# Performance work log

Measured on AMD Instinct MI355X. Metric: run time of the kernel, lower is better.

The kernel has to match this reference:

```python
import jax, jax.numpy as jnp
import numpy as np

EPS = 1e-5

def _hdc_branch(emb, w, b, dil, ln_g, ln_b):
    # emb: [N, L, E]; w: [K, E, F] ('WIO'); same-length dilated conv
    y = jax.lax.conv_general_dilated(
        emb, w, window_strides=(1,), padding=[(dil, dil)],
        rhs_dilation=(dil,), dimension_numbers=('NWC', 'WIO', 'NWC')) + b
    m = y.mean(-1, keepdims=True)
    v = ((y - m) ** 2).mean(-1, keepdims=True)
    y = (y - m) / jnp.sqrt(v + EPS) * ln_g + ln_b
    return jax.nn.relu(y)  # [N, L, F]

def _news_encoder(titles, embedding, w1, b1, w2, b2, w3, b3, ln_g, ln_b,
                  q_levels, q_words):
    B, n, L = titles.shape
    E = embedding.shape[-1]
    emb = embedding[titles].reshape(B * n, L, E)  # dropout = identity (eval)
    d = jnp.stack([
        _hdc_branch(emb, w1, b1, 1, ln_g, ln_b),
        _hdc_branch(emb, w2, b2, 2, ln_g, ln_b),
        _hdc_branch(emb, w3, b3, 3, ln_g, ln_b),
    ], axis=2)  # [Bn, L, 3, F]
    F = d.shape[-1]
    d = d.reshape(B, n, L, 3, F)
    scale = jnp.sqrt(jnp.asarray(E, d.dtype))  # original divides by sqrt(embedding_dim)
    # level-wise attention pooling (1-row query over 3 levels)
    wl = jax.nn.softmax(jnp.einsum('f,bnlkf->bnlk', q_levels[0], d) / scale, axis=-1)
    attn = jnp.einsum('bnlk,bnlkf->bnlf', wl, d)  # [B, n, L, F]
    # word-wise attention pooling (1-row query over L words)
    ww = jax.nn.softmax(jnp.einsum('f,bnlf->bnl', q_words[0], attn) / scale, axis=-1)
    reprs = jnp.einsum('bnl,bnlf->bnf', ww, attn)  # [B, n, F]
    return reprs

def setup_inputs() -> dict:
    key = jax.random.key(0)
    ks = jax.random.split(key, 12)
    V, E, F, H = 50000, 300, 150, 50
    return {
        'candidate_title': jax.random.randint(ks[0], (64, 5, 30), 0, V),
        'clicked_title': jax.random.randint(ks[1], (64, H, 30), 0, V),
        'embedding': jax.random.normal(ks[2], (V, E), jnp.float32),
        'w1': jax.random.normal(ks[3], (3, E, F), jnp.float32) * 0.05,
        'b1': jax.random.normal(ks[4], (F,), jnp.float32) * 0.05,
        'w2': jax.random.normal(ks[5], (3, E, F), jnp.float32) * 0.05,
        'b2': jax.random.normal(ks[6], (F,), jnp.float32) * 0.05,
        'w3': jax.random.normal(ks[7], (3, E, F), jnp.float32) * 0.05,
        'b3': jax.random.normal(ks[8], (F,), jnp.float32) * 0.05,
        'ln_g': jnp.ones((F,), jnp.float32),
        'ln_b': jnp.zeros((F,), jnp.float32),
        'q_levels': jax.random.normal(ks[9], (1, F), jnp.float32),
        'q_words': jax.random.normal(ks[10], (1, F), jnp.float32),
        'ltr_w': jax.random.normal(ks[11], (1, H), jnp.float32) * 0.1,
        'ltr_b': jnp.zeros((1,), jnp.float32),
    }

def reference(candidate_title, clicked_title, embedding, w1, b1, w2, b2, w3, b3,
              ln_g, ln_b, q_levels, q_words, ltr_w, ltr_b):
    cdd = _news_encoder(candidate_title, embedding, w1, b1, w2, b2, w3, b3,
                        ln_g, ln_b, q_levels, q_words)  # [B, cdd, F]
    his = _news_encoder(clicked_title, embedding, w1, b1, w2, b2, w3, b3,
                        ln_g, ln_b, q_levels, q_words)  # [B, his, F]
    scores = jnp.einsum('bcf,bhf->bch', cdd, his)        # [B, cdd, his]
    logits = jnp.einsum('bch,oh->bco', scores, ltr_w)[..., 0] + ltr_b[0]  # [B, cdd]
    return jax.nn.log_softmax(logits, axis=1)  # cdd_size > 1 branch
```

## Files before the change

### kernel.cpp

```cpp
#include <hip/hip_runtime.h>

typedef unsigned short u16;
typedef unsigned int   u32;
typedef __bf16 bf16x8 __attribute__((ext_vector_type(8)));
typedef float  f32x4  __attribute__((ext_vector_type(4)));
typedef _Float16 h2 __attribute__((ext_vector_type(2)));

#define M_ROWS 50000
#define M_PAD  50176
#define M_TILES 196
#define N_REAL 1368
#define N_PAD  1536
#define N_TILES64 22
#define K_DIM  300
#define K_PAD  320
#define KT     10
#define TROW   1408
#define SEG    152
#define YCOL   152

#define GLDS(gp, lp) __builtin_amdgcn_global_load_lds( \
    (const __attribute__((address_space(1))) void*)(gp), \
    (__attribute__((address_space(3))) void*)(lp), 16, 0, 0)

static __device__ __forceinline__ u16 f2bf(float x){
  union { float f; u32 u; } a; a.f = x;
  u32 r = a.u + 0x7fffu + ((a.u >> 16) & 1u);
  return (u16)(r >> 16);
}
static __device__ __forceinline__ u16 f2h(float x){
  _Float16 h = (_Float16)x;
  u16 r; __builtin_memcpy(&r, &h, 2); return r;
}
static __device__ __forceinline__ float h2f(u16 v){
  _Float16 h; __builtin_memcpy(&h, &v, 2); return (float)h;
}

static __device__ __forceinline__ float wsum63(float x){
  asm volatile(
    "s_nop 1\n\t"
    "v_add_f32 %0, %0, %0 row_shr:1 bound_ctrl:0\n\t"
    "s_nop 1\n\t"
    "v_add_f32 %0, %0, %0 row_shr:2 bound_ctrl:0\n\t"
    "s_nop 1\n\t"
    "v_add_f32 %0, %0, %0 row_shr:4 bound_ctrl:0\n\t"
    "s_nop 1\n\t"
    "v_add_f32 %0, %0, %0 row_shr:8 bound_ctrl:0\n\t"
    "s_nop 1\n\t"
    "v_add_f32 %0, %0, %0 row_bcast:15 row_mask:0xa\n\t"
    "s_nop 1\n\t"
    "v_add_f32 %0, %0, %0 row_bcast:31 row_mask:0xc\n\t"
    "s_nop 1"
    : "+v"(x));
  return x;
}
static __device__ __forceinline__ float wmax63(float x){
  asm volatile(
    "s_nop 1\n\t"
    "v_max_f32 %0, %0, %0 row_shr:1\n\t"
    "s_nop 1\n\t"
    "v_max_f32 %0, %0, %0 row_shr:2\n\t"
    "s_nop 1\n\t"
    "v_max_f32 %0, %0, %0 row_shr:4\n\t"
    "s_nop 1\n\t"
    "v_max_f32 %0, %0, %0 row_shr:8\n\t"
    "s_nop 1\n\t"
    "v_max_f32 %0, %0, %0 row_bcast:15 row_mask:0xa\n\t"
    "s_nop 1\n\t"
    "v_max_f32 %0, %0, %0 row_bcast:31 row_mask:0xc\n\t"
    "s_nop 1"
    : "+v"(x));
  return x;
}
static __device__ __forceinline__ float rdl63(float x){
  union { float f; int i; } a; a.f = x;
  union { int i; float f; } r; r.i = __builtin_amdgcn_readlane(a.i, 63);
  return r.f;
}

__global__ __launch_bounds__(256) void build_A(const float* __restrict__ emb, u16* __restrict__ A){
  int t = blockIdx.x * 256 + threadIdx.x;
  if (t >= M_PAD * 40) return;
  int m = t / 40, kg = t % 40;
  int k0 = kg * 8;
  int kt = kg >> 2, kgl = kg & 3;
  int tile = m >> 8, ml = m & 255, mb = ml >> 4, row = ml & 15;
  size_t off = ((size_t)tile * KT + kt) * 8192 + mb * 512 + kgl * 128 + row * 8;
  union { uint4 q; u16 s[8]; } p;
  if (m < M_ROWS && k0 + 8 <= K_DIM){
    const float4* src = (const float4*)(emb + (size_t)m * K_DIM + k0);
    float4 v0 = src[0], v1 = src[1];
    p.s[0] = f2bf(v0.x); p.s[1] = f2bf(v0.y); p.s[2] = f2bf(v0.z); p.s[3] = f2bf(v0.w);
    p.s[4] = f2bf(v1.x); p.s[5] = f2bf(v1.y); p.s[6] = f2bf(v1.z); p.s[7] = f2bf(v1.w);
  } else {
    #pragma unroll
    for (int j = 0; j < 8; ++j){
      int k = k0 + j;
      float x = (m < M_ROWS && k < K_DIM) ? emb[(size_t)m * K_DIM + k] : 0.f;
      p.s[j] = f2bf(x);
    }
  }
  *(uint4*)(A + off) = p.q;
}

__global__ void build_B(const float* __restrict__ w1, const float* __restrict__ w2,
                        const float* __restrict__ w3, u16* __restrict__ B){
  int t = blockIdx.x * 256 + threadIdx.x;
  if (t >= N_PAD * K_PAD) return;
  int n = t / K_PAD, k = t % K_PAD;
  float x = 0.f;
  if (n < N_REAL && k < K_DIM){
    int br = n / 456, rem = n % 456, tap = rem / 152, f = rem % 152;
    if (f < 150){
      const float* w = (br == 0) ? w1 : ((br == 1) ? w2 : w3);
      x = w[(tap * K_DIM + k) * 150 + f];
    }
  }
  int tn = n >> 7, nl = n & 127, nb = nl >> 4, col = nl & 15;
  int kt = k >> 5, kl = k & 31, kg = kl >> 3, k8 = kl & 7;
  B[((size_t)tn * KT + kt) * 4096 + nb * 512 + kg * 128 + col * 8 + k8] = f2bf(x);
}

__global__ __launch_bounds__(256, 5) void gemm_k(const u16* __restrict__ A, const u16* __restrict__ B,
                                                 u16* __restrict__ T){
  __shared__ __align__(16) u16 lds[6144];
  const int flat = blockIdx.x;
  const int xcd = flat & 7, ord = flat >> 3;
  const int wg = xcd * 1078 + ord;
  const int tn = wg % 22, tM = wg / 22;
  const int t256 = tM >> 1, hM = tM & 1;
  const int tn128 = tn >> 1, h64 = tn & 1;
  const int tid = threadIdx.x, wave = tid >> 6, lane = tid & 63;
  const int wm = wave >> 1, wn = wave & 1;
  f32x4 acc[4][2];
  #pragma unroll
  for (int i = 0; i < 4; ++i)
    #pragma unroll
    for (int j = 0; j < 2; ++j) acc[i][j] = (f32x4){0.f, 0.f, 0.f, 0.f};
  const u16* Ab = A + ((size_t)t256 * KT) * 8192 + hM * 4096;
  const u16* Bb = B + ((size_t)tn128 * KT) * 4096 + h64 * 2048;
  #pragma unroll
  for (int s = 0; s < 10; ++s){
    __syncthreads();
    GLDS(Ab + s * 8192 + tid * 8,        lds + tid * 8);
    GLDS(Ab + s * 8192 + 2048 + tid * 8, lds + 2048 + tid * 8);
    GLDS(Bb + s * 4096 + tid * 8,        lds + 4096 + tid * 8);
    __syncthreads();
    const bf16x8* A8 = (const bf16x8*)lds;
    const bf16x8* B8 = (const bf16x8*)(lds + 4096);
    bf16x8 av[4], bv[2];
    #pragma unroll
    for (int i = 0; i < 4; ++i) av[i] = A8[(wm * 4 + i) * 64 + lane];
    #pragma unroll
    for (int j = 0; j < 2; ++j) bv[j] = B8[(wn * 2 + j) * 64 + lane];
    #pragma unroll
    for (int i = 0; i < 4; ++i)
      #pragma unroll
      for (int j = 0; j < 2; ++j)
        acc[i][j] = __builtin_amdgcn_mfma_f32_16x16x32_bf16(av[i], bv[j], acc[i][j], 0, 0, 0);
  }
  const int r0 = (lane >> 4) * 4, c0 = lane & 15;
  const int row = tid >> 2, q = tid & 3;
  #pragma unroll
  for (int h = 0; h < 2; ++h){
    __syncthreads();
    if (wm == h){
      #pragma unroll
      for (int i = 0; i < 4; ++i){
        #pragma unroll
        for (int j = 0; j < 2; ++j){
          int col = wn * 32 + j * 16 + c0;
          #pragma unroll
          for (int r = 0; r < 4; ++r)
            lds[(i * 16 + r0 + r) * 72 + col] = f2h(acc[i][j][r]);
        }
      }
    }
    __syncthreads();
    int m = tM * 128 + h * 64 + row;
    if (m < M_ROWS){
      const u16* src = lds + row * 72 + q * 16;
      u16* dst = T + (size_t)m * TROW + tn * 64 + q * 16;
      *(uint4*)(dst)     = *(const uint4*)(src);
      *(uint4*)(dst + 8) = *(const uint4*)(src + 8);
    }
  }
}

__global__ __launch_bounds__(512, 4) void encode_k(
    const int* __restrict__ cand, const int* __restrict__ clk,
    const u16* __restrict__ T,
    const float* __restrict__ b1, const float* __restrict__ b2, const float* __restrict__ b3,
    const float* __restrict__ lng, const float* __restrict__ lnb,
    const float* __restrict__ ql, const float* __restrict__ qw,
    float* __restrict__ rc, float* __restrict__ rh){
  __shared__ __align__(16) u16 ybuf[90][YCOL];
  __shared__ float tl[32];
  __shared__ float pbuf[8][YCOL];
  __shared__ u32 wordoff[32];
  const int t = blockIdx.x;
  const int tid = threadIdx.x, wave = tid >> 6, lane = tid & 63;
  const int* wp; float* outp;
  if (t < 320){ wp = cand + t * 30;                outp = rc + t * 150; }
  else        { wp = clk + (size_t)(t - 320) * 30; outp = rh + (size_t)(t - 320) * 150; }
  if (tid < 30) wordoff[tid] = (u32)wp[tid] * (u32)TROW;
  __syncthreads();
  const float invs = 0.057735026918962576f;
  const int f0 = lane, f1 = lane + 64, f2 = lane + 128;
  const bool has2 = (f2 < 150);

  uint4 rv[12]; bool vm[12]; int pA[4], fgA[4]; bool ivA[4];
  #pragma unroll
  for (int it = 0; it < 4; ++it){
    const int item = tid + it * 512;
    const bool iv = item < 1710;
    const int p = item / 19, fg = item - p * 19;
    pA[it] = p; fgA[it] = fg; ivA[it] = iv;
    const int l = p / 3, br = p - l * 3, dil = br + 1;
    #pragma unroll
    for (int tap = 0; tap < 3; ++tap){
      const int ls = l + (tap - 1) * dil;
      const int lsc = ls < 0 ? 0 : (ls > 29 ? 29 : ls);
      vm[it * 3 + tap] = iv && (ls >= 0) && (ls < 30);
      rv[it * 3 + tap] = *(const uint4*)(T + wordoff[lsc] + br * 456 + tap * SEG + fg * 8);
    }
  }
  #pragma unroll
  for (int it = 0; it < 4; ++it){
    if (ivA[it]){
      union { uint4 q; h2 h[4]; } s, va, vb, vc;
      const uint4 z4 = (uint4){0u, 0u, 0u, 0u};
      va.q = vm[it * 3]     ? rv[it * 3]     : z4;
      vb.q = vm[it * 3 + 1] ? rv[it * 3 + 1] : z4;
      vc.q = vm[it * 3 + 2] ? rv[it * 3 + 2] : z4;
      #pragma unroll
      for (int i = 0; i < 4; ++i) s.h[i] = va.h[i] + vb.h[i] + vc.h[i];
      *(uint4*)&ybuf[pA[it]][fgA[it] * 8] = s.q;
    }
  }

  float qlv0 = ql[f0], qlv1 = ql[f1], qlv2 = has2 ? ql[f2] : 0.f;
  float qwv0 = qw[f0], qwv1 = qw[f1], qwv2 = has2 ? qw[f2] : 0.f;
  float lg0 = lng[f0], lg1 = lng[f1], lg2 = has2 ? lng[f2] : 0.f;
  float lb0 = lnb[f0], lb1 = lnb[f1], lb2 = has2 ? lnb[f2] : 0.f;
  float bs[3][3];
  {
    const float* bl[3] = {b1, b2, b3};
    #pragma unroll
    for (int br = 0; br < 3; ++br){
      bs[br][0] = bl[br][f0]; bs[br][1] = bl[br][f1]; bs[br][2] = has2 ? bl[br][f2] : 0.f;
    }
  }
  __syncthreads();

  float at0[4], at1[4], at2[4];
  #pragma unroll
  for (int q = 0; q < 4; ++q){
    const int l = wave + q * 8;
    at0[q] = 0.f; at1[q] = 0.f; at2[q] = 0.f;
    if (l < 30){
      float dr[3][3]; float lvl[3];
      #pragma unroll
      for (int br = 0; br < 3; ++br){
        int p = l * 3 + br;
        float y0 = h2f(ybuf[p][f0]) + bs[br][0];
        float y1 = h2f(ybuf[p][f1]) + bs[br][1];
        float y2 = has2 ? (h2f(ybuf[p][f2]) + bs[br][2]) : 0.f;
        float s  = y0 + y1 + y2;
        float ss = y0 * y0 + y1 * y1 + y2 * y2;
        float st = wsum63(s), sst = wsum63(ss);
        float mean = rdl63(st) * (1.f / 150.f);
        float var  = rdl63(sst) * (1.f / 150.f) - mean * mean;
        float rstd = rsqrtf(var + 1e-5f);
        float d0 = fmaxf((y0 - mean) * rstd * lg0 + lb0, 0.f);
        float d1 = fmaxf((y1 - mean) * rstd * lg1 + lb1, 0.f);
        float d2 = has2 ? fmaxf((y2 - mean) * rstd * lg2 + lb2, 0.f) : 0.f;
        dr[br][0] = d0; dr[br][1] = d1; dr[br][2] = d2;
        float dot = qlv0 * d0 + qlv1 * d1 + qlv2 * d2;
        lvl[br] = rdl63(wsum63(dot)) * invs;
      }
      float mx = fmaxf(lvl[0], fmaxf(lvl[1], lvl[2]));
      float e0 = __expf(lvl[0] - mx), e1 = __expf(lvl[1] - mx), e2 = __expf(lvl[2] - mx);
      float inv = 1.f / (e0 + e1 + e2);
      float w0 = e0 * inv, w1v = e1 * inv, w2v = e2 * inv;
      float a0 = w0 * dr[0][0] + w1v * dr[1][0] + w2v * dr[2][0];
      float a1 = w0 * dr[0][1] + w1v * dr[1][1] + w2v * dr[2][1];
      float a2 = w0 * dr[0][2] + w1v * dr[1][2] + w2v * dr[2][2];
      float dot = qwv0 * a0 + qwv1 * a1 + qwv2 * a2;
      float tw = wsum63(dot);
      if (lane == 63) tl[l] = tw * invs;
      at0[q] = a0; at1[q] = a1; at2[q] = a2;
    }
  }
  __syncthreads();

  if (wave == 0){
    float v = (lane < 30) ? tl[lane] : -1e30f;
    float mx = rdl63(wmax63(v));
    float e = (lane < 30) ? __expf(v - mx) : 0.f;
    float den = rdl63(wsum63(e));
    if (lane < 30) tl[lane] = e / den;
  }
  __syncthreads();

  float p0 = 0.f, p1 = 0.f, p2 = 0.f;
  #pragma unroll
  for (int q = 0; q < 4; ++q){
    const int l = wave + q * 8;
    if (l < 30){
      float wwv = tl[l];
      p0 += wwv * at0[q]; p1 += wwv * at1[q]; p2 += wwv * at2[q];
    }
  }
  pbuf[wave][lane] = p0;
  pbuf[wave][lane + 64] = p1;
  if (has2) pbuf[wave][lane + 128] = p2;
  __syncthreads();
  if (tid < 150){
    float acc = 0.f;
    #pragma unroll
    for (int w = 0; w < 8; ++w) acc += pbuf[w][tid];
    outp[tid] = acc;
  }
}

__global__ __launch_bounds__(256) void final_k(const float* __restrict__ rc, const float* __restrict__ rh,
                                               const float* __restrict__ lw, const float* __restrict__ lb,
                                               float* __restrict__ out){
  __shared__ float Cl[750];
  __shared__ float Hl[7500];
  __shared__ float sc[5][52];
  __shared__ float lg[5];
  const int b = blockIdx.x, tid = threadIdx.x;
  const float* C = rc + b * 750;
  const float* H = rh + (size_t)b * 7500;
  for (int i = tid; i < 750; i += 256) Cl[i] = C[i];
  for (int i = tid; i < 7500; i += 256) Hl[i] = H[i];
  __syncthreads();
  if (tid < 250){
    int c = tid / 50, h = tid % 50;
    float s = 0.f;
    #pragma unroll 10
    for (int k = 0; k < 150; ++k) s += Cl[c * 150 + k] * Hl[h * 150 + k];
    sc[c][h] = s;
  }
  __syncthreads();
  if (tid < 5){
    float s = lb[0];
    for (int h = 0; h < 50; ++h) s += sc[tid][h] * lw[h];
    lg[tid] = s;
  }
  __syncthreads();
  if (tid < 5){
    float mx = fmaxf(fmaxf(fmaxf(lg[0], lg[1]), fmaxf(lg[2], lg[3])), lg[4]);
    float den = 0.f;
    for (int c = 0; c < 5; ++c) den += expf(lg[c] - mx);
    out[b * 5 + tid] = lg[tid] - mx - logf(den);
  }
}

extern "C" void kernel_launch(void* const* d_in, const int* in_sizes, int n_in,
                              void* d_out, int out_size, void* d_ws, size_t ws_size,
                              hipStream_t stream){
  const int*   cand = (const int*)d_in[0];
  const int*   clk  = (const int*)d_in[1];
  const float* emb  = (const float*)d_in[2];
  const float* w1   = (const float*)d_in[3];
  const float* b1   = (const float*)d_in[4];
  const float* w2   = (const float*)d_in[5];
  const float* b2   = (const float*)d_in[6];
  const float* w3   = (const float*)d_in[7];
  const float* b3   = (const float*)d_in[8];
  const float* lng  = (const float*)d_in[9];
  const float* lnb  = (const float*)d_in[10];
  const float* ql   = (const float*)d_in[11];
  const float* qw   = (const float*)d_in[12];
  const float* lw   = (const float*)d_in[13];
  const float* lb   = (const float*)d_in[14];
  float* out = (float*)d_out;

  char* ws = (char*)d_ws;
  const size_t szA = (size_t)M_TILES * KT * 16384;
  const size_t szB = (size_t)12 * KT * 8192;
  const size_t szT = (size_t)M_ROWS * TROW * 2;
  u16*   A  = (u16*)ws;
  u16*   B  = (u16*)(ws + szA);
  u16*   T  = (u16*)(ws + szA + szB);
  float* rc = (float*)(ws + szA + szB + szT);
  float* rh = rc + 320 * 150;

  build_A<<<(M_PAD * 40 + 255) / 256, 256, 0, stream>>>(emb, A);
  build_B<<<(N_PAD * K_PAD + 255) / 256, 256, 0, stream>>>(w1, w2, w3, B);
  gemm_k<<<dim3(392 * N_TILES64), 256, 0, stream>>>(A, B, T);
  encode_k<<<3520, 512, 0, stream>>>(cand, clk, T, b1, b2, b3, lng, lnb, ql, qw, rc, rh);
  final_k<<<64, 256, 0, stream>>>(rc, rh, lw, lb, out);
}
```

Measured before the change: 260.1 us.

## Double-buffer GEMM LDS loads and stage build_A through shared memory

The GEMM main loop now prefetches the next K-slice into a second LDS buffer with global_load_lds while computing the current one. It uses explicit vmcnt waits and raw s_barriers instead of two __syncthreads per step, and raises the occupancy hint from 5 to 6. build_A is restructured so each block handles one 256x32 tile, reads coalesced float4 rows, permutes them in LDS, and writes contiguous 16-byte chunks. This aims to hide global load latency in the GEMM and fix scattered writes in the layout kernel, at the cost of doubled LDS per GEMM block and hand-managed waitcnt correctness.

```diff
diff --git a/kernel.cpp b/kernel.cpp
--- a/kernel.cpp
+++ b/kernel.cpp
@@ -79,28 +79,31 @@
 }
 
 __global__ __launch_bounds__(256) void build_A(const float* __restrict__ emb, u16* __restrict__ A){
-  int t = blockIdx.x * 256 + threadIdx.x;
-  if (t >= M_PAD * 40) return;
-  int m = t / 40, kg = t % 40;
-  int k0 = kg * 8;
-  int kt = kg >> 2, kgl = kg & 3;
-  int tile = m >> 8, ml = m & 255, mb = ml >> 4, row = ml & 15;
-  size_t off = ((size_t)tile * KT + kt) * 8192 + mb * 512 + kgl * 128 + row * 8;
-  union { uint4 q; u16 s[8]; } p;
-  if (m < M_ROWS && k0 + 8 <= K_DIM){
-    const float4* src = (const float4*)(emb + (size_t)m * K_DIM + k0);
-    float4 v0 = src[0], v1 = src[1];
-    p.s[0] = f2bf(v0.x); p.s[1] = f2bf(v0.y); p.s[2] = f2bf(v0.z); p.s[3] = f2bf(v0.w);
-    p.s[4] = f2bf(v1.x); p.s[5] = f2bf(v1.y); p.s[6] = f2bf(v1.z); p.s[7] = f2bf(v1.w);
-  } else {
-    #pragma unroll
-    for (int j = 0; j < 8; ++j){
-      int k = k0 + j;
-      float x = (m < M_ROWS && k < K_DIM) ? emb[(size_t)m * K_DIM + k] : 0.f;
-      p.s[j] = f2bf(x);
-    }
-  }
-  *(uint4*)(A + off) = p.q;
+  __shared__ __align__(16) u16 st[8192];
+  const int blk = blockIdx.x;
+  const int tile = blk / KT, kt = blk % KT;
+  const int tid = threadIdx.x;
+  const int m0 = tile * 256, k0 = kt * 32;
+  #pragma unroll
+  for (int u = 0; u < 8; ++u){
+    int i = tid + u * 256;
+    int r = i >> 3, c = i & 7;
+    int m = m0 + r, k = k0 + c * 4;
+    float4 v = (float4){0.f, 0.f, 0.f, 0.f};
+    if (m < M_ROWS && k < K_DIM)
+      v = *(const float4*)(emb + (size_t)m * K_DIM + k);
+    int dst = (r >> 4) * 512 + (c >> 1) * 128 + (r & 15) * 8 + (c & 1) * 4;
+    union { u32 d[2]; u16 s[4]; } w;
+    w.s[0] = f2bf(v.x); w.s[1] = f2bf(v.y); w.s[2] = f2bf(v.z); w.s[3] = f2bf(v.w);
+    *(uint2*)(st + dst) = *(const uint2*)w.d;
+  }
+  __syncthreads();
+  u16* out = A + ((size_t)tile * KT + kt) * 8192;
+  #pragma unroll
+  for (int q = 0; q < 4; ++q){
+    int o = tid * 8 + q * 2048;
+    *(uint4*)(out + o) = *(const uint4*)(st + o);
+  }
 }
 
 __global__ void build_B(const float* __restrict__ w1, const float* __restrict__ w2,
@@ -121,9 +124,9 @@
   B[((size_t)tn * KT + kt) * 4096 + nb * 512 + kg * 128 + col * 8 + k8] = f2bf(x);
 }
 
-__global__ __launch_bounds__(256, 5) void gemm_k(const u16* __restrict__ A, const u16* __restrict__ B,
+__global__ __launch_bounds__(256, 6) void gemm_k(const u16* __restrict__ A, const u16* __restrict__ B,
                                                  u16* __restrict__ T){
-  __shared__ __align__(16) u16 lds[6144];
+  __shared__ __align__(16) u16 lds[12288];
   const int flat = blockIdx.x;
   const int xcd = flat & 7, ord = flat >> 3;
   const int wg = xcd * 1078 + ord;
@@ -139,15 +142,26 @@
     for (int j = 0; j < 2; ++j) acc[i][j] = (f32x4){0.f, 0.f, 0.f, 0.f};
   const u16* Ab = A + ((size_t)t256 * KT) * 8192 + hM * 4096;
   const u16* Bb = B + ((size_t)tn128 * KT) * 4096 + h64 * 2048;
+  GLDS(Ab + tid * 8,        lds + tid * 8);
+  GLDS(Ab + 2048 + tid * 8, lds + 2048 + tid * 8);
+  GLDS(Bb + tid * 8,        lds + 4096 + tid * 8);
   #pragma unroll
   for (int s = 0; s < 10; ++s){
-    __syncthreads();
-    GLDS(Ab + s * 8192 + tid * 8,        lds + tid * 8);
-    GLDS(Ab + s * 8192 + 2048 + tid * 8, lds + 2048 + tid * 8);
-    GLDS(Bb + s * 4096 + tid * 8,        lds + 4096 + tid * 8);
-    __syncthreads();
-    const bf16x8* A8 = (const bf16x8*)lds;
-    const bf16x8* B8 = (const bf16x8*)(lds + 4096);
+    const int b = s & 1;
+    u16* cur = lds + b * 6144;
+    if (s < 9){
+      u16* nxt = lds + (b ^ 1) * 6144;
+      GLDS(Ab + (s + 1) * 8192 + tid * 8,        nxt + tid * 8);
+      GLDS(Ab + (s + 1) * 8192 + 2048 + tid * 8, nxt + 2048 + tid * 8);
+      GLDS(Bb + (s + 1) * 4096 + tid * 8,        nxt + 4096 + tid * 8);
+      asm volatile("s_waitcnt vmcnt(3)" ::: "memory");
+    } else {
+      asm volatile("s_waitcnt vmcnt(0)" ::: "memory");
+    }
+    __builtin_amdgcn_sched_barrier(0);
+    __builtin_amdgcn_s_barrier();
+    const bf16x8* A8 = (const bf16x8*)cur;
+    const bf16x8* B8 = (const bf16x8*)(cur + 4096);
     bf16x8 av[4], bv[2];
     #pragma unroll
     for (int i = 0; i < 4; ++i) av[i] = A8[(wm * 4 + i) * 64 + lane];
@@ -158,6 +172,7 @@
       #pragma unroll
       for (int j = 0; j < 2; ++j)
         acc[i][j] = __builtin_amdgcn_mfma_f32_16x16x32_bf16(av[i], bv[j], acc[i][j], 0, 0, 0);
+    __builtin_amdgcn_s_barrier();
   }
   const int r0 = (lane >> 4) * 4, c0 = lane & 15;
   const int row = tid >> 2, q = tid & 3;
@@ -389,7 +404,7 @@
   float* rc = (float*)(ws + szA + szB + szT);
   float* rh = rc + 320 * 150;
 
-  build_A<<<(M_PAD * 40 + 255) / 256, 256, 0, stream>>>(emb, A);
+  build_A<<<M_TILES * KT, 256, 0, stream>>>(emb, A);
   build_B<<<(N_PAD * K_PAD + 255) / 256, 256, 0, stream>>>(w1, w2, w3, B);
   gemm_k<<<dim3(392 * N_TILES64), 256, 0, stream>>>(A, B, T);
   encode_k<<<3520, 512, 0, stream>>>(cand, clk, T, b1, b2, b3, lng, lnb, ql, qw, rc, rh);
```

New measurement: 254.9 us. -2.0%, faster.

## Fuse embedding bf16 conversion into GEMM A-tile loading

Applied to the files above, without the earlier changes.

Removes the separate build_A pass that converted the fp32 embedding table into a tiled bf16 buffer. The GEMM now loads fp32 embedding rows directly, converts them to bf16 in registers and stores them into the LDS tile layout, while B still uses global_load_lds. This removes one kernel launch and a full write/read of the converted A matrix, but each N-tile block now re-reads twice as many bytes of A with synchronous loads. Occupancy hint raised to 8 blocks per CU.

```diff
diff --git a/kernel.cpp b/kernel.cpp
--- a/kernel.cpp
+++ b/kernel.cpp
@@ -78,33 +78,10 @@
   return r.f;
 }
 
-__global__ __launch_bounds__(256) void build_A(const float* __restrict__ emb, u16* __restrict__ A){
-  int t = blockIdx.x * 256 + threadIdx.x;
-  if (t >= M_PAD * 40) return;
-  int m = t / 40, kg = t % 40;
-  int k0 = kg * 8;
-  int kt = kg >> 2, kgl = kg & 3;
-  int tile = m >> 8, ml = m & 255, mb = ml >> 4, row = ml & 15;
-  size_t off = ((size_t)tile * KT + kt) * 8192 + mb * 512 + kgl * 128 + row * 8;
-  union { uint4 q; u16 s[8]; } p;
-  if (m < M_ROWS && k0 + 8 <= K_DIM){
-    const float4* src = (const float4*)(emb + (size_t)m * K_DIM + k0);
-    float4 v0 = src[0], v1 = src[1];
-    p.s[0] = f2bf(v0.x); p.s[1] = f2bf(v0.y); p.s[2] = f2bf(v0.z); p.s[3] = f2bf(v0.w);
-    p.s[4] = f2bf(v1.x); p.s[5] = f2bf(v1.y); p.s[6] = f2bf(v1.z); p.s[7] = f2bf(v1.w);
-  } else {
-    #pragma unroll
-    for (int j = 0; j < 8; ++j){
-      int k = k0 + j;
-      float x = (m < M_ROWS && k < K_DIM) ? emb[(size_t)m * K_DIM + k] : 0.f;
-      p.s[j] = f2bf(x);
-    }
-  }
-  *(uint4*)(A + off) = p.q;
-}
-
-__global__ void build_B(const float* __restrict__ w1, const float* __restrict__ w2,
-                        const float* __restrict__ w3, u16* __restrict__ B){
+__global__ __launch_bounds__(256) void build_B(const float* __restrict__ w1,
+                                               const float* __restrict__ w2,
+                                               const float* __restrict__ w3,
+                                               u16* __restrict__ B){
   int t = blockIdx.x * 256 + threadIdx.x;
   if (t >= N_PAD * K_PAD) return;
   int n = t / K_PAD, k = t % K_PAD;
@@ -121,14 +98,14 @@
   B[((size_t)tn * KT + kt) * 4096 + nb * 512 + kg * 128 + col * 8 + k8] = f2bf(x);
 }
 
-__global__ __launch_bounds__(256, 5) void gemm_k(const u16* __restrict__ A, const u16* __restrict__ B,
+__global__ __launch_bounds__(256, 8) void gemm_k(const float* __restrict__ emb,
+                                                 const u16* __restrict__ B,
                                                  u16* __restrict__ T){
   __shared__ __align__(16) u16 lds[6144];
   const int flat = blockIdx.x;
   const int xcd = flat & 7, ord = flat >> 3;
   const int wg = xcd * 1078 + ord;
   const int tn = wg % 22, tM = wg / 22;
-  const int t256 = tM >> 1, hM = tM & 1;
   const int tn128 = tn >> 1, h64 = tn & 1;
   const int tid = threadIdx.x, wave = tid >> 6, lane = tid & 63;
   const int wm = wave >> 1, wn = wave & 1;
@@ -137,14 +114,34 @@
   for (int i = 0; i < 4; ++i)
     #pragma unroll
     for (int j = 0; j < 2; ++j) acc[i][j] = (f32x4){0.f, 0.f, 0.f, 0.f};
-  const u16* Ab = A + ((size_t)t256 * KT) * 8192 + hM * 4096;
   const u16* Bb = B + ((size_t)tn128 * KT) * 4096 + h64 * 2048;
+  const int r0i = (tid >> 1);
   #pragma unroll
   for (int s = 0; s < 10; ++s){
     __syncthreads();
-    GLDS(Ab + s * 8192 + tid * 8,        lds + tid * 8);
-    GLDS(Ab + s * 8192 + 2048 + tid * 8, lds + 2048 + tid * 8);
-    GLDS(Bb + s * 4096 + tid * 8,        lds + 4096 + tid * 8);
+    GLDS(Bb + s * 4096 + tid * 8, lds + 4096 + tid * 8);
+    #pragma unroll
+    for (int it = 0; it < 2; ++it){
+      const int r = (tid >> 2) + it * 64;
+      const int kgl = tid & 3;
+      const int m = tM * 128 + r;
+      const int k0 = s * 32 + kgl * 8;
+      union { uint4 q; u16 h[8]; } o;
+      if (m < M_ROWS && k0 + 8 <= K_DIM){
+        const float4* src = (const float4*)(emb + (size_t)m * K_DIM + k0);
+        float4 v0 = src[0], v1 = src[1];
+        o.h[0] = f2bf(v0.x); o.h[1] = f2bf(v0.y); o.h[2] = f2bf(v0.z); o.h[3] = f2bf(v0.w);
+        o.h[4] = f2bf(v1.x); o.h[5] = f2bf(v1.y); o.h[6] = f2bf(v1.z); o.h[7] = f2bf(v1.w);
+      } else {
+        #pragma unroll
+        for (int j = 0; j < 8; ++j){
+          int k = k0 + j;
+          float x = (m < M_ROWS && k < K_DIM) ? emb[(size_t)m * K_DIM + k] : 0.f;
+          o.h[j] = f2bf(x);
+        }
+      }
+      *(uint4*)(lds + (r >> 4) * 512 + kgl * 128 + (r & 15) * 8) = o.q;
+    }
     __syncthreads();
     const bf16x8* A8 = (const bf16x8*)lds;
     const bf16x8* B8 = (const bf16x8*)(lds + 4096);
@@ -159,7 +156,8 @@
       for (int j = 0; j < 2; ++j)
         acc[i][j] = __builtin_amdgcn_mfma_f32_16x16x32_bf16(av[i], bv[j], acc[i][j], 0, 0, 0);
   }
-  const int r0 = (lane >> 4) * 4, c0 = lane & 15;
+  (void)r0i;
+  const int rr0 = (lane >> 4) * 4, c0 = lane & 15;
   const int row = tid >> 2, q = tid & 3;
   #pragma unroll
   for (int h = 0; h < 2; ++h){
@@ -172,7 +170,7 @@
           int col = wn * 32 + j * 16 + c0;
           #pragma unroll
           for (int r = 0; r < 4; ++r)
-            lds[(i * 16 + r0 + r) * 72 + col] = f2h(acc[i][j][r]);
+            lds[(i * 16 + rr0 + r) * 72 + col] = f2h(acc[i][j][r]);
         }
       }
     }
@@ -380,18 +378,15 @@
   float* out = (float*)d_out;
 
   char* ws = (char*)d_ws;
-  const size_t szA = (size_t)M_TILES * KT * 16384;
   const size_t szB = (size_t)12 * KT * 8192;
   const size_t szT = (size_t)M_ROWS * TROW * 2;
-  u16*   A  = (u16*)ws;
-  u16*   B  = (u16*)(ws + szA);
-  u16*   T  = (u16*)(ws + szA + szB);
-  float* rc = (float*)(ws + szA + szB + szT);
+  u16*   B  = (u16*)ws;
+  u16*   T  = (u16*)(ws + szB);
+  float* rc = (float*)(ws + szB + szT);
   float* rh = rc + 320 * 150;
 
-  build_A<<<(M_PAD * 40 + 255) / 256, 256, 0, stream>>>(emb, A);
   build_B<<<(N_PAD * K_PAD + 255) / 256, 256, 0, stream>>>(w1, w2, w3, B);
-  gemm_k<<<dim3(392 * N_TILES64), 256, 0, stream>>>(A, B, T);
+  gemm_k<<<dim3(392 * N_TILES64), 256, 0, stream>>>(emb, B, T);
   encode_k<<<3520, 512, 0, stream>>>(cand, clk, T, b1, b2, b3, lng, lnb, ql, qw, rc, rh);
   final_k<<<64, 256, 0, stream>>>(rc, rh, lw, lb, out);
 }
```

New measurement: 371.5 us. +42.8%, slower.
